# Performance work log

Measured on AMD Instinct MI355X. Metric: run time of the kernel, lower is better.

The kernel has to match this reference:

```python
import jax, jax.numpy as jnp
import numpy as np

N_ATOMS = 10000
N_EDGES = 250000
F_DIM = 128
N_RBF = 20
CUTOFF = 5.0
N_INT = 3
EPS = 1e-8


def setup_inputs() -> dict:
    key = jax.random.key(0)
    ks = jax.random.split(key, 16)
    inp = {}
    inp["atomic_numbers"] = jax.random.randint(ks[0], (N_ATOMS,), 1, 101)
    # positions in a 5 Angstrom box so many pairs lie inside the cutoff
    inp["R"] = jax.random.uniform(ks[1], (N_ATOMS, 3), dtype=jnp.float32) * 5.0
    idx_i = jnp.sort(jax.random.randint(ks[2], (N_EDGES,), 0, N_ATOMS))
    # ensure idx_j != idx_i so d_ij > 0
    idx_j = (idx_i + 1 + jax.random.randint(ks[3], (N_EDGES,), 0, N_ATOMS - 1)) % N_ATOMS
    inp["idx_i"] = idx_i
    inp["idx_j"] = idx_j
    inp["offsets"] = jnp.zeros((N_EDGES, 3), dtype=jnp.float32)

    def w(k, shape):
        fan_in = shape[-2]
        return jax.random.normal(k, shape, dtype=jnp.float32) / np.sqrt(fan_in).astype(np.float32)

    inp["emb"] = jax.random.normal(ks[4], (101, F_DIM), dtype=jnp.float32)
    inp["filt_W"] = w(ks[5], (N_RBF, 3 * F_DIM))
    inp["filt_b"] = jax.random.normal(ks[6], (3 * F_DIM,), dtype=jnp.float32) * 0.01
    inp["int_W1"] = w(ks[7], (N_INT, F_DIM, F_DIM))
    inp["int_b1"] = jnp.zeros((N_INT, 1, F_DIM), dtype=jnp.float32)
    inp["int_W2"] = w(ks[8], (N_INT, F_DIM, 3 * F_DIM))
    inp["int_b2"] = jnp.zeros((N_INT, 1, 3 * F_DIM), dtype=jnp.float32)
    inp["mix_Wmu"] = w(ks[9], (N_INT, F_DIM, 2 * F_DIM))
    inp["mix_W1"] = w(ks[10], (N_INT, 2 * F_DIM, F_DIM))
    inp["mix_b1"] = jnp.zeros((N_INT, 1, F_DIM), dtype=jnp.float32)
    inp["mix_W2"] = w(ks[11], (N_INT, F_DIM, 3 * F_DIM))
    inp["mix_b2"] = jnp.zeros((N_INT, 1, 3 * F_DIM), dtype=jnp.float32)
    return inp


def painn_forward(atomic_numbers, idx_i, idx_j, R, offsets, emb, filt_W, filt_b,
                  int_W1, int_b1, int_W2, int_b2,
                  mix_Wmu, mix_W1, mix_b1, mix_W2, mix_b2):
    n_atoms = atomic_numbers.shape[0]
    # geometry
    r_ij = R[idx_j] - R[idx_i] + offsets                      # [E,3]
    d_ij = jnp.linalg.norm(r_ij, axis=1, keepdims=True)       # [E,1]
    dir_ij = r_ij / d_ij                                      # [E,3]
    # Gaussian radial basis + cosine cutoff (schnetpack defaults)
    centers = jnp.linspace(0.0, CUTOFF, N_RBF, dtype=jnp.float32)
    coeff = -0.5 / (centers[1] - centers[0]) ** 2
    phi = jnp.exp(coeff * (d_ij[..., None] - centers) ** 2)   # [E,1,N_RBF]
    fcut = 0.5 * (jnp.cos(d_ij * (jnp.pi / CUTOFF)) + 1.0) * (d_ij < CUTOFF)  # [E,1]
    Wij = (phi @ filt_W + filt_b) * fcut[..., None]           # [E,1,3F] (shared filters)

    q = emb[atomic_numbers][:, None, :]                       # [N,1,F]
    mu = jnp.zeros((n_atoms, 3, F_DIM), dtype=q.dtype)        # [N,3,F]

    for i in range(N_INT):
        # ---- interaction (equivariant message passing) ----
        x = jax.nn.silu(q @ int_W1[i] + int_b1[i]) @ int_W2[i] + int_b2[i]  # [N,1,3F]
        xj = x[idx_j]                                          # [E,1,3F]
        muj = mu[idx_j]                                        # [E,3,F]
        xw = Wij * xj                                          # [E,1,3F]
        dq, dmuR, dmumu = jnp.split(xw, 3, axis=-1)            # each [E,1,F]
        dq = jax.ops.segment_sum(dq, idx_i, num_segments=n_atoms)          # [N,1,F]
        dmu = dmuR * dir_ij[..., None] + dmumu * muj           # [E,3,F]
        dmu = jax.ops.segment_sum(dmu, idx_i, num_segments=n_atoms)        # [N,3,F]
        q = q + dq
        mu = mu + dmu
        # ---- mixing (intra-atomic) ----
        mu_mix = mu @ mix_Wmu[i]                               # [N,3,2F]
        mu_V, mu_W = jnp.split(mu_mix, 2, axis=-1)             # [N,3,F] each
        mu_Vn = jnp.sqrt(jnp.sum(mu_V ** 2, axis=-2, keepdims=True) + EPS)  # [N,1,F]
        ctx = jnp.concatenate([q, mu_Vn], axis=-1)             # [N,1,2F]
        xm = jax.nn.silu(ctx @ mix_W1[i] + mix_b1[i]) @ mix_W2[i] + mix_b2[i]  # [N,1,3F]
        dq_intra, dmu_intra, dqmu_intra = jnp.split(xm, 3, axis=-1)
        dmu_intra = dmu_intra * mu_W                           # [N,3,F]
        dqmu_intra = dqmu_intra * jnp.sum(mu_V * mu_W, axis=1, keepdims=True)  # [N,1,F]
        q = q + dq_intra + dqmu_intra
        mu = mu + dmu_intra

    return q.squeeze(1), mu                                    # [N,F], [N,3,F]


def reference(atomic_numbers, R, idx_i, idx_j, offsets, emb, filt_W, filt_b,
              int_W1, int_b1, int_W2, int_b2,
              mix_Wmu, mix_W1, mix_b1, mix_W2, mix_b2):
    return painn_forward(atomic_numbers, idx_i, idx_j, R, offsets, emb, filt_W, filt_b,
                         int_W1, int_b1, int_W2, int_b2,
                         mix_Wmu, mix_W1, mix_b1, mix_W2, mix_b2)
```

## Files before the change

### kernel.cpp

```cpp
#include <hip/hip_runtime.h>
#include <math.h>

#define NA 10000
#define NE 250000
#define FD 128
#define NRBF 20
#define RCUT 5.0f

typedef _Float16 h16;
typedef __attribute__((ext_vector_type(8))) _Float16 half8;
typedef __attribute__((ext_vector_type(2))) _Float16 half2v;
typedef __attribute__((ext_vector_type(4))) float f32x4;

static __device__ __forceinline__ half8 f32x8_to_h8(const float* p) {
    float4 a = *(const float4*)p;
    float4 b = *(const float4*)(p + 4);
    half8 r;
    r[0] = (h16)a.x; r[1] = (h16)a.y; r[2] = (h16)a.z; r[3] = (h16)a.w;
    r[4] = (h16)b.x; r[5] = (h16)b.y; r[6] = (h16)b.z; r[7] = (h16)b.w;
    return r;
}
static __device__ __forceinline__ float silu(float v) {
    return v / (1.f + expf(-v));
}

__global__ __launch_bounds__(256) void setup_kernel(
    const float* __restrict__ R, const int* __restrict__ idx_i,
    const int* __restrict__ idx_j, const float* __restrict__ offsets,
    float* __restrict__ dir, h16* __restrict__ ph, int* __restrict__ row_start,
    const float* __restrict__ int_W1, const float* __restrict__ int_W2,
    const float* __restrict__ mix_Wmu, const float* __restrict__ mix_W1,
    const float* __restrict__ mix_W2,
    h16* __restrict__ W1t, h16* __restrict__ W2t, h16* __restrict__ WmuT,
    h16* __restrict__ mW1t, h16* __restrict__ mW2t,
    const float* __restrict__ filt_W, const float* __restrict__ filt_b,
    h16* __restrict__ fwt)
{
    const int b = blockIdx.x;
    if (b < 977) {
        int e = b * 256 + threadIdx.x;
        if (e >= NE) return;
        int i = idx_i[e], j = idx_j[e];
        float rx = R[j * 3 + 0] - R[i * 3 + 0] + offsets[e * 3 + 0];
        float ry = R[j * 3 + 1] - R[i * 3 + 1] + offsets[e * 3 + 1];
        float rz = R[j * 3 + 2] - R[i * 3 + 2] + offsets[e * 3 + 2];
        float d = sqrtf(rx * rx + ry * ry + rz * rz);
        float inv = 1.f / d;
        float fcut = 0.f;
        if (d < RCUT) fcut = 0.5f * (cosf(d * (3.14159265358979323846f / RCUT)) + 1.f);
        *(float4*)&dir[(size_t)e * 4] = make_float4(rx * inv, ry * inv, rz * inv, 0.f);
        h16* pp = ph + (size_t)e * 32;
        const float delta = RCUT / 19.f;
        const float coeff = -0.5f / (delta * delta);
#pragma unroll
        for (int r = 0; r < NRBF; ++r) {
            float dc = d - (float)r * delta;
            pp[r] = (h16)(expf(coeff * dc * dc) * fcut);
        }
        pp[20] = (h16)fcut;
#pragma unroll
        for (int r = 21; r < 32; ++r) pp[r] = (h16)0.f;
    } else if (b < 1017) {
        int n = (b - 977) * 256 + threadIdx.x;
        if (n > NA) return;
        int lo = 0, hi = NE;
        while (lo < hi) {
            int mid = (lo + hi) >> 1;
            if (idx_i[mid] < n) lo = mid + 1; else hi = mid;
        }
        row_start[n] = lo;
    } else {
        int idx = (b - 1017) * 256 + threadIdx.x;
        if (idx < 49152) {
            int bt = idx >> 14, rem = idx & 16383;
            int nn = rem >> 7, kk = rem & 127;
            W1t[idx] = (h16)int_W1[(size_t)bt * 16384 + kk * 128 + nn];
        } else if ((idx -= 49152) < 147456) {
            int bt = idx / 49152, rem = idx - bt * 49152;
            int nn = rem >> 7, kk = rem & 127;
            W2t[idx] = (h16)int_W2[(size_t)bt * 49152 + kk * 384 + nn];
        } else if ((idx -= 147456) < 98304) {
            int bt = idx >> 15, rem = idx & 32767;
            int nn = rem >> 7, kk = rem & 127;
            WmuT[idx] = (h16)mix_Wmu[(size_t)bt * 32768 + kk * 256 + nn];
        } else if ((idx -= 98304) < 98304) {
            int bt = idx >> 15, rem = idx & 32767;
            int nn = rem >> 8, kk = rem & 255;
            mW1t[idx] = (h16)mix_W1[(size_t)bt * 32768 + kk * 128 + nn];
        } else if ((idx -= 98304) < 147456) {
            int bt = idx / 49152, rem = idx - bt * 49152;
            int nn = rem >> 7, kk = rem & 127;
            mW2t[idx] = (h16)mix_W2[(size_t)bt * 49152 + kk * 384 + nn];
        } else if ((idx -= 147456) < 12288) {
            int nn = idx >> 5, kk = idx & 31;
            float v = 0.f;
            if (kk < 20) v = filt_W[kk * 384 + nn];
            else if (kk == 20) v = filt_b[nn];
            fwt[idx] = (h16)v;
        }
    }
}

__global__ __launch_bounds__(256) void intmlp0_kernel(
    const int* __restrict__ Z, const float* __restrict__ emb, float* __restrict__ q,
    const h16* __restrict__ W1t, const float* __restrict__ b1,
    const h16* __restrict__ W2t, const float* __restrict__ b2, h16* __restrict__ x16)
{
    __shared__ h16 Hs[16 * 136];
    const int tid = threadIdx.x;
    const int wave = tid >> 6, lane = tid & 63;
    const int ar = lane & 15, kg = lane >> 4;
    const size_t row0 = (size_t)blockIdx.x * 16;

    {
        int a = tid >> 4, f0 = (tid & 15) * 8;
        const float* src = emb + (size_t)Z[row0 + a] * 128 + f0;
        float4 v0 = *(const float4*)src;
        float4 v1 = *(const float4*)(src + 4);
        *(float4*)&q[(row0 + a) * 128 + f0] = v0;
        *(float4*)&q[(row0 + a) * 128 + f0 + 4] = v1;
    }
    const int zr = Z[row0 + ar];
    f32x4 a1[2] = {};
    for (int ks = 0; ks < 128; ks += 32) {
        int k = ks + kg * 8;
        half8 af = f32x8_to_h8(emb + (size_t)zr * 128 + k);
#pragma unroll
        for (int tt = 0; tt < 2; ++tt) {
            int t = wave * 2 + tt;
            half8 bf = *(const half8*)&W1t[(size_t)(t * 16 + ar) * 128 + k];
            a1[tt] = __builtin_amdgcn_mfma_f32_16x16x32_f16(af, bf, a1[tt], 0, 0, 0);
        }
    }
#pragma unroll
    for (int tt = 0; tt < 2; ++tt) {
        int col = (wave * 2 + tt) * 16 + ar;
        float bb = b1[col];
#pragma unroll
        for (int r = 0; r < 4; ++r)
            Hs[(kg * 4 + r) * 136 + col] = (h16)silu(a1[tt][r] + bb);
    }
    __syncthreads();
    f32x4 a2[6] = {};
    for (int ks = 0; ks < 128; ks += 32) {
        int k = ks + kg * 8;
        half8 af = *(const half8*)&Hs[ar * 136 + k];
#pragma unroll
        for (int tt = 0; tt < 6; ++tt) {
            int t = wave * 6 + tt;
            half8 bf = *(const half8*)&W2t[(size_t)(t * 16 + ar) * 128 + k];
            a2[tt] = __builtin_amdgcn_mfma_f32_16x16x32_f16(af, bf, a2[tt], 0, 0, 0);
        }
    }
#pragma unroll
    for (int tt = 0; tt < 6; ++tt) {
        int col = (wave * 6 + tt) * 16 + ar;
        float bb = b2[col];
#pragma unroll
        for (int r = 0; r < 4; ++r)
            x16[(row0 + kg * 4 + r) * 384 + col] = (h16)(a2[tt][r] + bb);
    }
}

template<bool HAS_MU>
__global__ __launch_bounds__(128) void edge_kernel(
    const float* __restrict__ dir, const h16* __restrict__ ph,
    const h16* __restrict__ fwt,
    const int* __restrict__ row_start, const int* __restrict__ idx_j,
    const h16* __restrict__ x16, const h16* __restrict__ mu16p,
    const float* __restrict__ mup, float* __restrict__ mun,
    h16* __restrict__ mu16n, float* __restrict__ q)
{
    const int n = blockIdx.x, f = threadIdx.x;
    half2v fa[12], fb[12], fc[12];
    {
        const half8* pa = (const half8*)(fwt + (size_t)f * 32);
        const half8* pb = (const half8*)(fwt + (size_t)(128 + f) * 32);
#pragma unroll
        for (int r = 0; r < 3; ++r) {
            *(half8*)&fa[r * 4] = pa[r];
            *(half8*)&fb[r * 4] = pb[r];
        }
        if (HAS_MU) {
            const half8* pc = (const half8*)(fwt + (size_t)(256 + f) * 32);
#pragma unroll
            for (int r = 0; r < 3; ++r)
                *(half8*)&fc[r * 4] = pc[r];
        }
    }
    float accq = 0.f, am0 = 0.f, am1 = 0.f, am2 = 0.f;
    const int e0 = row_start[n], e1 = row_start[n + 1];
    for (int e = e0; e < e1; ++e) {
        half2v pr[12];
        const h16* pb8 = ph + (size_t)e * 32;
        *(half8*)&pr[0] = *(const half8*)pb8;
        *(half8*)&pr[4] = *(const half8*)(pb8 + 8);
        *(half8*)&pr[8] = *(const half8*)(pb8 + 16);
        half2v A0 = {(h16)0.f, (h16)0.f}, A1 = A0, A2 = A0;
#pragma unroll
        for (int r = 0; r < 11; ++r) {
            A0 = pr[r] * fa[r] + A0;
            A1 = pr[r] * fb[r] + A1;
            if (HAS_MU) A2 = pr[r] * fc[r] + A2;
        }
        float w0 = (float)A0[0] + (float)A0[1];
        float w1 = (float)A1[0] + (float)A1[1];
        int j = idx_j[e];
        float4 g = *(const float4*)&dir[(size_t)e * 4];
        const h16* xb = x16 + (size_t)j * 384;
        float x0 = (float)xb[f], x1 = (float)xb[128 + f];
        accq = fmaf(w0, x0, accq);
        float xw1 = w1 * x1;
        if (HAS_MU) {
            float w2 = (float)A2[0] + (float)A2[1];
            float x2 = (float)xb[256 + f];
            float xw2 = w2 * x2;
            const h16* mb = mu16p + (size_t)j * 384;
            am0 += xw1 * g.x + xw2 * (float)mb[f];
            am1 += xw1 * g.y + xw2 * (float)mb[128 + f];
            am2 += xw1 * g.z + xw2 * (float)mb[256 + f];
        } else {
            am0 = fmaf(xw1, g.x, am0);
            am1 = fmaf(xw1, g.y, am1);
            am2 = fmaf(xw1, g.z, am2);
        }
    }
    q[(size_t)n * FD + f] += accq;
    size_t b = (size_t)n * 384;
    float m0 = (HAS_MU ? mup[b + f] : 0.f) + am0;
    float m1 = (HAS_MU ? mup[b + 128 + f] : 0.f) + am1;
    float m2 = (HAS_MU ? mup[b + 256 + f] : 0.f) + am2;
    mun[b + f] = m0; mun[b + 128 + f] = m1; mun[b + 256 + f] = m2;
    mu16n[b + f] = (h16)m0; mu16n[b + 128 + f] = (h16)m1; mu16n[b + 256 + f] = (h16)m2;
}

__global__ __launch_bounds__(256) void mixint_kernel(
    const h16* __restrict__ mu16n, const h16* __restrict__ WmuT,
    const h16* __restrict__ W1t, const float* __restrict__ b1,
    const h16* __restrict__ W2t, const float* __restrict__ b2,
    float* __restrict__ q, float* __restrict__ mu, h16* __restrict__ mu16w,
    const h16* __restrict__ nW1t, const float* __restrict__ nb1,
    const h16* __restrict__ nW2t, const float* __restrict__ nb2,
    h16* __restrict__ x16)
{
    __shared__ h16 MM[48 * 264];
    __shared__ h16 CT[16 * 264];
    __shared__ h16 Hs[16 * 136];
    __shared__ h16 XM[16 * 392];
    const int tid = threadIdx.x;
    const int wave = tid >> 6, lane = tid & 63;
    const int ar = lane & 15, kg = lane >> 4;
    const size_t row0 = (size_t)blockIdx.x * 16;

    {
        f32x4 acc[3][4] = {};
        int aloc[3], dloc[3];
#pragma unroll
        for (int rt = 0; rt < 3; ++rt) {
            int rr = rt * 16 + ar;
            aloc[rt] = rr / 3;
            dloc[rt] = rr - 3 * aloc[rt];
        }
        for (int ks = 0; ks < 128; ks += 32) {
            int k = ks + kg * 8;
            half8 afr[3];
#pragma unroll
            for (int rt = 0; rt < 3; ++rt)
                afr[rt] = *(const half8*)&mu16n[(row0 + aloc[rt]) * 384 + dloc[rt] * 128 + k];
#pragma unroll
            for (int ct = 0; ct < 4; ++ct) {
                int cc = wave * 4 + ct;
                half8 bf = *(const half8*)&WmuT[(size_t)(cc * 16 + ar) * 128 + k];
#pragma unroll
                for (int rt = 0; rt < 3; ++rt)
                    acc[rt][ct] = __builtin_amdgcn_mfma_f32_16x16x32_f16(afr[rt], bf, acc[rt][ct], 0, 0, 0);
            }
        }
#pragma unroll
        for (int rt = 0; rt < 3; ++rt)
#pragma unroll
            for (int ct = 0; ct < 4; ++ct) {
                int col = (wave * 4 + ct) * 16 + ar;
#pragma unroll
                for (int r = 0; r < 4; ++r)
                    MM[(rt * 16 + kg * 4 + r) * 264 + col] = (h16)acc[rt][ct][r];
            }
    }
    __syncthreads();

    {
        int a = tid >> 4, fi = (tid & 15) * 8;
        const float* qp = q + (row0 + a) * 128 + fi;
        float4 q0 = *(const float4*)qp;
        float4 q1 = *(const float4*)(qp + 4);
        float qv[8] = {q0.x, q0.y, q0.z, q0.w, q1.x, q1.y, q1.z, q1.w};
#pragma unroll
        for (int jj = 0; jj < 8; ++jj) {
            int ff = fi + jj;
            float v0 = (float)MM[(a * 3 + 0) * 264 + ff];
            float v1 = (float)MM[(a * 3 + 1) * 264 + ff];
            float v2 = (float)MM[(a * 3 + 2) * 264 + ff];
            CT[a * 264 + 128 + ff] = (h16)sqrtf(v0 * v0 + v1 * v1 + v2 * v2 + 1e-8f);
            CT[a * 264 + ff] = (h16)qv[jj];
        }
    }
    __syncthreads();

    {
        f32x4 a1[2] = {};
        for (int ks = 0; ks < 256; ks += 32) {
            int k = ks + kg * 8;
            half8 af = *(const half8*)&CT[ar * 264 + k];
#pragma unroll
            for (int tt = 0; tt < 2; ++tt) {
                int t = wave * 2 + tt;
                half8 bf = *(const half8*)&W1t[(size_t)(t * 16 + ar) * 256 + k];
                a1[tt] = __builtin_amdgcn_mfma_f32_16x16x32_f16(af, bf, a1[tt], 0, 0, 0);
            }
        }
#pragma unroll
        for (int tt = 0; tt < 2; ++tt) {
            int col = (wave * 2 + tt) * 16 + ar;
            float bb = b1[col];
#pragma unroll
            for (int r = 0; r < 4; ++r)
                Hs[(kg * 4 + r) * 136 + col] = (h16)silu(a1[tt][r] + bb);
        }
    }
    __syncthreads();

    {
        f32x4 a2[6] = {};
        for (int ks = 0; ks < 128; ks += 32) {
            int k = ks + kg * 8;
            half8 af = *(const half8*)&Hs[ar * 136 + k];
#pragma unroll
            for (int tt = 0; tt < 6; ++tt) {
                int t = wave * 6 + tt;
                half8 bf = *(const half8*)&W2t[(size_t)(t * 16 + ar) * 128 + k];
                a2[tt] = __builtin_amdgcn_mfma_f32_16x16x32_f16(af, bf, a2[tt], 0, 0, 0);
            }
        }
#pragma unroll
        for (int tt = 0; tt < 6; ++tt) {
            int col = (wave * 6 + tt) * 16 + ar;
            float bb = b2[col];
#pragma unroll
            for (int r = 0; r < 4; ++r)
                XM[(kg * 4 + r) * 392 + col] = (h16)(a2[tt][r] + bb);
        }
    }
    __syncthreads();

    {
        int a = tid >> 4, fi = (tid & 15) * 8;
        size_t n = row0 + a;
#pragma unroll
        for (int jj = 0; jj < 8; ++jj) {
            int ff = fi + jj;
            float dq  = (float)XM[a * 392 + ff];
            float dm  = (float)XM[a * 392 + 128 + ff];
            float dqm = (float)XM[a * 392 + 256 + ff];
            float v0 = (float)MM[(a * 3 + 0) * 264 + ff], w0 = (float)MM[(a * 3 + 0) * 264 + 128 + ff];
            float v1 = (float)MM[(a * 3 + 1) * 264 + ff], w1 = (float)MM[(a * 3 + 1) * 264 + 128 + ff];
            float v2 = (float)MM[(a * 3 + 2) * 264 + ff], w2 = (float)MM[(a * 3 + 2) * 264 + 128 + ff];
            float sv = v0 * w0 + v1 * w1 + v2 * w2;
            float qn = q[n * 128 + ff] + dq + dqm * sv;
            q[n * 128 + ff] = qn;
            CT[a * 264 + ff] = (h16)qn;
            size_t b = n * 384 + ff;
            float m0 = mu[b] + dm * w0;
            float m1 = mu[b + 128] + dm * w1;
            float m2 = mu[b + 256] + dm * w2;
            mu[b] = m0; mu[b + 128] = m1; mu[b + 256] = m2;
            mu16w[b] = (h16)m0; mu16w[b + 128] = (h16)m1; mu16w[b + 256] = (h16)m2;
        }
    }
    if (!nW1t) return;
    __syncthreads();

    {
        f32x4 a1[2] = {};
        for (int ks = 0; ks < 128; ks += 32) {
            int k = ks + kg * 8;
            half8 af = *(const half8*)&CT[ar * 264 + k];
#pragma unroll
            for (int tt = 0; tt < 2; ++tt) {
                int t = wave * 2 + tt;
                half8 bf = *(const half8*)&nW1t[(size_t)(t * 16 + ar) * 128 + k];
                a1[tt] = __builtin_amdgcn_mfma_f32_16x16x32_f16(af, bf, a1[tt], 0, 0, 0);
            }
        }
#pragma unroll
        for (int tt = 0; tt < 2; ++tt) {
            int col = (wave * 2 + tt) * 16 + ar;
            float bb = nb1[col];
#pragma unroll
            for (int r = 0; r < 4; ++r)
                Hs[(kg * 4 + r) * 136 + col] = (h16)silu(a1[tt][r] + bb);
        }
        __syncthreads();
        f32x4 a2[6] = {};
        for (int ks = 0; ks < 128; ks += 32) {
            int k = ks + kg * 8;
            half8 af = *(const half8*)&Hs[ar * 136 + k];
#pragma unroll
            for (int tt = 0; tt < 6; ++tt) {
                int t = wave * 6 + tt;
                half8 bf = *(const half8*)&nW2t[(size_t)(t * 16 + ar) * 128 + k];
                a2[tt] = __builtin_amdgcn_mfma_f32_16x16x32_f16(af, bf, a2[tt], 0, 0, 0);
            }
        }
#pragma unroll
        for (int tt = 0; tt < 6; ++tt) {
            int col = (wave * 6 + tt) * 16 + ar;
            float bb = nb2[col];
#pragma unroll
            for (int r = 0; r < 4; ++r)
                x16[(row0 + kg * 4 + r) * 384 + col] = (h16)(a2[tt][r] + bb);
        }
    }
}

extern "C" void kernel_launch(void* const* d_in, const int* in_sizes, int n_in,
                              void* d_out, int out_size, void* d_ws, size_t ws_size,
                              hipStream_t stream)
{
    const int*   Z       = (const int*)d_in[0];
    const float* R       = (const float*)d_in[1];
    const int*   idx_i   = (const int*)d_in[2];
    const int*   idx_j   = (const int*)d_in[3];
    const float* offsets = (const float*)d_in[4];
    const float* emb     = (const float*)d_in[5];
    const float* filt_W  = (const float*)d_in[6];
    const float* filt_b  = (const float*)d_in[7];
    const float* int_W1  = (const float*)d_in[8];
    const float* int_b1  = (const float*)d_in[9];
    const float* int_W2  = (const float*)d_in[10];
    const float* int_b2  = (const float*)d_in[11];
    const float* mix_Wmu = (const float*)d_in[12];
    const float* mix_W1  = (const float*)d_in[13];
    const float* mix_b1  = (const float*)d_in[14];
    const float* mix_W2  = (const float*)d_in[15];
    const float* mix_b2  = (const float*)d_in[16];

    float* q_out  = (float*)d_out;
    float* mu_out = (float*)d_out + (size_t)NA * FD;

    char* base = (char*)d_ws;
    size_t o = 0;
    auto alloc = [&](size_t bytes) -> void* {
        void* p = base + o;
        o += (bytes + 255) & ~(size_t)255;
        return p;
    };
    float* dir    = (float*)alloc((size_t)NE * 4 * 4);
    h16*   ph     = (h16*)alloc((size_t)NE * 32 * 2);
    h16*   x16    = (h16*)alloc((size_t)NA * 384 * 2);
    h16*   mu16a  = (h16*)alloc((size_t)NA * 384 * 2);
    h16*   mu16b  = (h16*)alloc((size_t)NA * 384 * 2);
    float* mu_ws  = (float*)alloc((size_t)NA * 384 * 4);
    h16*   W1t    = (h16*)alloc((size_t)3 * 128 * 128 * 2);
    h16*   W2t    = (h16*)alloc((size_t)3 * 384 * 128 * 2);
    h16*   WmuT   = (h16*)alloc((size_t)3 * 256 * 128 * 2);
    h16*   mW1t   = (h16*)alloc((size_t)3 * 128 * 256 * 2);
    h16*   mW2t   = (h16*)alloc((size_t)3 * 384 * 128 * 2);
    h16*   fwt    = (h16*)alloc((size_t)384 * 32 * 2);
    int*   row_st = (int*)alloc((size_t)(NA + 1) * 4);

    setup_kernel<<<3177, 256, 0, stream>>>(R, idx_i, idx_j, offsets, dir, ph, row_st,
                                           int_W1, int_W2, mix_Wmu, mix_W1, mix_W2,
                                           W1t, W2t, WmuT, mW1t, mW2t,
                                           filt_W, filt_b, fwt);

    intmlp0_kernel<<<NA / 16, 256, 0, stream>>>(Z, emb, q_out,
                                                W1t, int_b1, W2t, int_b2, x16);
    edge_kernel<false><<<NA, 128, 0, stream>>>(dir, ph, fwt, row_st, idx_j,
                                               x16, nullptr, nullptr, mu_out, mu16b, q_out);
    mixint_kernel<<<NA / 16, 256, 0, stream>>>(
        mu16b, WmuT, mW1t, mix_b1, mW2t, mix_b2, q_out, mu_out, mu16b,
        W1t + 16384, int_b1 + 128, W2t + 49152, int_b2 + 384, x16);

    edge_kernel<true><<<NA, 128, 0, stream>>>(dir, ph, fwt, row_st, idx_j,
                                              x16, mu16b, mu_out, mu_ws, mu16a, q_out);
    mixint_kernel<<<NA / 16, 256, 0, stream>>>(
        mu16a, WmuT + 32768, mW1t + 32768, mix_b1 + 128, mW2t + 49152, mix_b2 + 384,
        q_out, mu_ws, mu16a,
        W1t + 32768, int_b1 + 256, W2t + 98304, int_b2 + 768, x16);

    edge_kernel<true><<<NA, 128, 0, stream>>>(dir, ph, fwt, row_st, idx_j,
                                              x16, mu16a, mu_ws, mu_out, mu16b, q_out);
    mixint_kernel<<<NA / 16, 256, 0, stream>>>(
        mu16b, WmuT + 65536, mW1t + 65536, mix_b1 + 256, mW2t + 98304, mix_b2 + 768,
        q_out, mu_out, mu16b,
        nullptr, nullptr, nullptr, nullptr, nullptr);
}
```

Before: 446.8 us.

## Interleave x and mu gather data per feature into one six-slot buffer

Replaces the separate x16 [N,384] and mu16 [N,384] neighbor buffers with one interleaved [N,128,6] fp16 layout. Each edge thread now gathers its x and mu values as three contiguous 32-bit loads instead of six scattered 16-bit loads. The neighbor loads are issued before the filter math so their latency overlaps it, and edge_kernel gets a min-waves launch bound. In exchange, the MLP and mix kernels write with a strided scatter, and the edge kernel's separate mu16 output becomes a buffer that the mix kernel reads and then rewrites into the interleaved slots.

```diff
diff --git a/kernel.cpp b/kernel.cpp
--- a/kernel.cpp
+++ b/kernel.cpp
@@ -104,7 +104,7 @@
 __global__ __launch_bounds__(256) void intmlp0_kernel(
     const int* __restrict__ Z, const float* __restrict__ emb, float* __restrict__ q,
     const h16* __restrict__ W1t, const float* __restrict__ b1,
-    const h16* __restrict__ W2t, const float* __restrict__ b2, h16* __restrict__ x16)
+    const h16* __restrict__ W2t, const float* __restrict__ b2, h16* __restrict__ xm)
 {
     __shared__ h16 Hs[16 * 136];
     const int tid = threadIdx.x;
@@ -156,20 +156,20 @@
     for (int tt = 0; tt < 6; ++tt) {
         int col = (wave * 6 + tt) * 16 + ar;
         float bb = b2[col];
+        int slot = col >> 7, ff = col & 127;
 #pragma unroll
         for (int r = 0; r < 4; ++r)
-            x16[(row0 + kg * 4 + r) * 384 + col] = (h16)(a2[tt][r] + bb);
+            xm[((size_t)(row0 + kg * 4 + r) * 128 + ff) * 6 + slot] = (h16)(a2[tt][r] + bb);
     }
 }
 
 template<bool HAS_MU>
-__global__ __launch_bounds__(128) void edge_kernel(
+__global__ __launch_bounds__(128, 5) void edge_kernel(
     const float* __restrict__ dir, const h16* __restrict__ ph,
     const h16* __restrict__ fwt,
     const int* __restrict__ row_start, const int* __restrict__ idx_j,
-    const h16* __restrict__ x16, const h16* __restrict__ mu16p,
-    const float* __restrict__ mup, float* __restrict__ mun,
-    h16* __restrict__ mu16n, float* __restrict__ q)
+    const h16* __restrict__ xm, const float* __restrict__ mup,
+    float* __restrict__ mun, h16* __restrict__ mu16n, float* __restrict__ q)
 {
     const int n = blockIdx.x, f = threadIdx.x;
     half2v fa[12], fb[12], fc[12];
@@ -188,14 +188,20 @@
                 *(half8*)&fc[r * 4] = pc[r];
         }
     }
+    const h16* xmf = xm + (size_t)f * 6;
     float accq = 0.f, am0 = 0.f, am1 = 0.f, am2 = 0.f;
     const int e0 = row_start[n], e1 = row_start[n + 1];
     for (int e = e0; e < e1; ++e) {
+        int j = idx_j[e];
+        const unsigned int* gp = (const unsigned int*)(xmf + (size_t)j * 768);
+        unsigned int g0 = gp[0], g1 = gp[1], g2 = 0u;
+        if (HAS_MU) g2 = gp[2];
         half2v pr[12];
         const h16* pb8 = ph + (size_t)e * 32;
         *(half8*)&pr[0] = *(const half8*)pb8;
         *(half8*)&pr[4] = *(const half8*)(pb8 + 8);
         *(half8*)&pr[8] = *(const half8*)(pb8 + 16);
+        float4 g = *(const float4*)&dir[(size_t)e * 4];
         half2v A0 = {(h16)0.f, (h16)0.f}, A1 = A0, A2 = A0;
 #pragma unroll
         for (int r = 0; r < 11; ++r) {
@@ -205,20 +211,19 @@
         }
         float w0 = (float)A0[0] + (float)A0[1];
         float w1 = (float)A1[0] + (float)A1[1];
-        int j = idx_j[e];
-        float4 g = *(const float4*)&dir[(size_t)e * 4];
-        const h16* xb = x16 + (size_t)j * 384;
-        float x0 = (float)xb[f], x1 = (float)xb[128 + f];
+        half2v h01 = __builtin_bit_cast(half2v, g0);
+        half2v h23 = __builtin_bit_cast(half2v, g1);
+        float x0 = (float)h01[0], x1 = (float)h01[1];
         accq = fmaf(w0, x0, accq);
         float xw1 = w1 * x1;
         if (HAS_MU) {
             float w2 = (float)A2[0] + (float)A2[1];
-            float x2 = (float)xb[256 + f];
+            half2v h45 = __builtin_bit_cast(half2v, g2);
+            float x2 = (float)h23[0];
             float xw2 = w2 * x2;
-            const h16* mb = mu16p + (size_t)j * 384;
-            am0 += xw1 * g.x + xw2 * (float)mb[f];
-            am1 += xw1 * g.y + xw2 * (float)mb[128 + f];
-            am2 += xw1 * g.z + xw2 * (float)mb[256 + f];
+            am0 += xw1 * g.x + xw2 * (float)h23[1];
+            am1 += xw1 * g.y + xw2 * (float)h45[0];
+            am2 += xw1 * g.z + xw2 * (float)h45[1];
         } else {
             am0 = fmaf(xw1, g.x, am0);
             am1 = fmaf(xw1, g.y, am1);
@@ -238,10 +243,9 @@
     const h16* __restrict__ mu16n, const h16* __restrict__ WmuT,
     const h16* __restrict__ W1t, const float* __restrict__ b1,
     const h16* __restrict__ W2t, const float* __restrict__ b2,
-    float* __restrict__ q, float* __restrict__ mu, h16* __restrict__ mu16w,
+    float* __restrict__ q, float* __restrict__ mu, h16* __restrict__ xmw,
     const h16* __restrict__ nW1t, const float* __restrict__ nb1,
-    const h16* __restrict__ nW2t, const float* __restrict__ nb2,
-    h16* __restrict__ x16)
+    const h16* __restrict__ nW2t, const float* __restrict__ nb2)
 {
     __shared__ h16 MM[48 * 264];
     __shared__ h16 CT[16 * 264];
@@ -373,7 +377,8 @@
             float m1 = mu[b + 128] + dm * w1;
             float m2 = mu[b + 256] + dm * w2;
             mu[b] = m0; mu[b + 128] = m1; mu[b + 256] = m2;
-            mu16w[b] = (h16)m0; mu16w[b + 128] = (h16)m1; mu16w[b + 256] = (h16)m2;
+            h16* xw = xmw + ((size_t)n * 128 + ff) * 6;
+            xw[3] = (h16)m0; xw[4] = (h16)m1; xw[5] = (h16)m2;
         }
     }
     if (!nW1t) return;
@@ -415,9 +420,10 @@
         for (int tt = 0; tt < 6; ++tt) {
             int col = (wave * 6 + tt) * 16 + ar;
             float bb = nb2[col];
+            int slot = col >> 7, ff = col & 127;
 #pragma unroll
             for (int r = 0; r < 4; ++r)
-                x16[(row0 + kg * 4 + r) * 384 + col] = (h16)(a2[tt][r] + bb);
+                xmw[((size_t)(row0 + kg * 4 + r) * 128 + ff) * 6 + slot] = (h16)(a2[tt][r] + bb);
         }
     }
 }
@@ -456,9 +462,8 @@
     };
     float* dir    = (float*)alloc((size_t)NE * 4 * 4);
     h16*   ph     = (h16*)alloc((size_t)NE * 32 * 2);
-    h16*   x16    = (h16*)alloc((size_t)NA * 384 * 2);
-    h16*   mu16a  = (h16*)alloc((size_t)NA * 384 * 2);
-    h16*   mu16b  = (h16*)alloc((size_t)NA * 384 * 2);
+    h16*   xm     = (h16*)alloc((size_t)NA * 128 * 6 * 2);
+    h16*   mu16p  = (h16*)alloc((size_t)NA * 384 * 2);
     float* mu_ws  = (float*)alloc((size_t)NA * 384 * 4);
     h16*   W1t    = (h16*)alloc((size_t)3 * 128 * 128 * 2);
     h16*   W2t    = (h16*)alloc((size_t)3 * 384 * 128 * 2);
@@ -474,24 +479,24 @@
                                            filt_W, filt_b, fwt);
 
     intmlp0_kernel<<<NA / 16, 256, 0, stream>>>(Z, emb, q_out,
-                                                W1t, int_b1, W2t, int_b2, x16);
+                                                W1t, int_b1, W2t, int_b2, xm);
     edge_kernel<false><<<NA, 128, 0, stream>>>(dir, ph, fwt, row_st, idx_j,
-                                               x16, nullptr, nullptr, mu_out, mu16b, q_out);
+                                               xm, nullptr, mu_out, mu16p, q_out);
     mixint_kernel<<<NA / 16, 256, 0, stream>>>(
-        mu16b, WmuT, mW1t, mix_b1, mW2t, mix_b2, q_out, mu_out, mu16b,
-        W1t + 16384, int_b1 + 128, W2t + 49152, int_b2 + 384, x16);
+        mu16p, WmuT, mW1t, mix_b1, mW2t, mix_b2, q_out, mu_out, xm,
+        W1t + 16384, int_b1 + 128, W2t + 49152, int_b2 + 384);
 
     edge_kernel<true><<<NA, 128, 0, stream>>>(dir, ph, fwt, row_st, idx_j,
-                                              x16, mu16b, mu_out, mu_ws, mu16a, q_out);
+                                              xm, mu_out, mu_ws, mu16p, q_out);
     mixint_kernel<<<NA / 16, 256, 0, stream>>>(
-        mu16a, WmuT + 32768, mW1t + 32768, mix_b1 + 128, mW2t + 49152, mix_b2 + 384,
-        q_out, mu_ws, mu16a,
-        W1t + 32768, int_b1 + 256, W2t + 98304, int_b2 + 768, x16);
+        mu16p, WmuT + 32768, mW1t + 32768, mix_b1 + 128, mW2t + 49152, mix_b2 + 384,
+        q_out, mu_ws, xm,
+        W1t + 32768, int_b1 + 256, W2t + 98304, int_b2 + 768);
 
     edge_kernel<true><<<NA, 128, 0, stream>>>(dir, ph, fwt, row_st, idx_j,
-                                              x16, mu16a, mu_ws, mu_out, mu16b, q_out);
+                                              xm, mu_ws, mu_out, mu16p, q_out);
     mixint_kernel<<<NA / 16, 256, 0, stream>>>(
-        mu16b, WmuT + 65536, mW1t + 65536, mix_b1 + 256, mW2t + 98304, mix_b2 + 768,
-        q_out, mu_out, mu16b,
-        nullptr, nullptr, nullptr, nullptr, nullptr);
-}
+        mu16p, WmuT + 65536, mW1t + 65536, mix_b1 + 256, mW2t + 98304, mix_b2 + 768,
+        q_out, mu_out, xm,
+        nullptr, nullptr, nullptr, nullptr);
+}
```

Result: slower. 493.7 us (+10.5%).
